# Kernel tuning notes

Hardware: AMD Instinct MI355X
Metric: run time of the kernel (lower is better)

## Reference

```python
import jax, jax.numpy as jnp
import numpy as np

N_MIN = 16
N_TABLES = 16
PER_LEVEL_SCALE = 1.3195079565048218
MAX_TABLE = 2 ** 19
H1, H2, H3 = 1, 2654435761, 805459861
OFFS = np.array([[0,0,0],[0,0,1],[0,1,0],[0,1,1],[1,0,0],[1,0,1],[1,1,0],[1,1,1]], dtype=np.int32)

def _levels():
    N_l, sizes, max_direct = [], [], 0
    for i in range(N_TABLES):
        res = int(np.ceil(N_MIN * np.exp(i * np.log(PER_LEVEL_SCALE)) - 1.0)) + 1
        ts = res ** 3
        ts = ts if ts % 8 == 0 else ((ts + 7) // 8) * 8
        ts = min(MAX_TABLE, ts)
        if ts == res ** 3:
            max_direct = i
        N_l.append(res); sizes.append(ts)
    return N_l, sizes, max_direct

N_L, SIZES, MAX_DIRECT = _levels()

def hash_encode(pos, grids):
    # pos: [N,3] in [0,1); grids: [16, MAX_TABLE, 2] (levels padded to MAX_TABLE)
    feats = []
    for l in range(N_TABLES):
        uvz = pos * jnp.float32(N_L[l])
        iuv_f = jnp.floor(uvz)
        f = uvz - iuv_f                                   # fractional part [N,3]
        corners = iuv_f.astype(jnp.int32)[:, None, :] + OFFS[None]  # [N,8,3]
        if l <= MAX_DIRECT:
            R = N_L[l]
            idx = (corners[..., 2] * (R * R) + corners[..., 1] * R + corners[..., 0]) % SIZES[l]
        else:
            cu = corners.astype(jnp.uint32)
            h = (cu[..., 0] * jnp.uint32(H1)) ^ (cu[..., 1] * jnp.uint32(H2)) ^ (cu[..., 2] * jnp.uint32(H3))
            idx = (h % jnp.uint32(SIZES[l])).astype(jnp.int32)
        c = grids[l][idx]                                 # gather -> [N,8,2]
        fx, fy, fz = f[:, 0:1], f[:, 1:2], f[:, 2:3]
        c00 = c[:, 0] * (1 - fx) + c[:, 4] * fx
        c01 = c[:, 1] * (1 - fx) + c[:, 5] * fx
        c10 = c[:, 2] * (1 - fx) + c[:, 6] * fx
        c11 = c[:, 3] * (1 - fx) + c[:, 7] * fx
        c0 = c00 * (1 - fy) + c10 * fy
        c1 = c01 * (1 - fy) + c11 * fy
        feats.append(c0 * (1 - fz) + c1 * fy)  # NOTE: c1*fy (not fz) replicates source exactly
    return jnp.concatenate(feats, axis=-1)  # [N, 32]

def setup_inputs():
    key = jax.random.key(0)
    ks = jax.random.split(key, 7)
    N = 1048576  # max_samples(512) * batch_size(2048)
    x = jax.random.uniform(ks[0], (N, 19), dtype=jnp.float32)  # pos(3) in [0,1) + dir feats(16)
    grids = (jax.random.uniform(ks[1], (N_TABLES, MAX_TABLE, 2), dtype=jnp.float32) * 2.0 - 1.0) * 1e-4
    h = 64
    w_sigma1 = jax.random.normal(ks[2], (32, h), dtype=jnp.float32) / np.sqrt(32).astype(np.float32)
    w_sigma2 = jax.random.normal(ks[3], (h, 16), dtype=jnp.float32) / np.sqrt(h).astype(np.float32)
    w_c1 = jax.random.normal(ks[4], (32, h), dtype=jnp.float32) / np.sqrt(32).astype(np.float32)
    w_c2 = jax.random.normal(ks[5], (h, h), dtype=jnp.float32) / np.sqrt(h).astype(np.float32)
    w_c3 = jax.random.normal(ks[6], (h, 3), dtype=jnp.float32) / np.sqrt(h).astype(np.float32)
    return {"x": x, "grids": grids, "w_sigma1": w_sigma1, "w_sigma2": w_sigma2,
            "w_c1": w_c1, "w_c2": w_c2, "w_c3": w_c3}

def reference(x, grids, w_sigma1, w_sigma2, w_c1, w_c2, w_c3):
    pos, direc = x[:, :3], x[:, 3:]
    enc = hash_encode(pos, grids)                       # [N,32]
    out = jax.nn.relu(enc @ w_sigma1) @ w_sigma2        # [N,16]
    sigma = out[:, 0]
    ci = jnp.concatenate([direc, out], axis=-1)         # [N,32]
    color = jax.nn.sigmoid(jax.nn.relu(jax.nn.relu(ci @ w_c1) @ w_c2) @ w_c3)  # [N,3]
    return jnp.concatenate([color, sigma[:, None]], axis=-1)  # [N,4]
```

## Files before the change

kernel.cpp:

```cpp
#include <hip/hip_runtime.h>
#include <math.h>


#define BLOCK 256
#define NTAB  (16*524288)
#define PITCH 88

constexpr int      kNL[16] = {16,22,28,37,49,65,85,112,148,195,257,338,446,589,777,1025};
constexpr unsigned kSZ[16] = {4096u,10648u,21952u,50656u,117656u,274632u,
                              524288u,524288u,524288u,524288u,524288u,
                              524288u,524288u,524288u,524288u,524288u};

typedef __attribute__((ext_vector_type(8))) short short8;
typedef __attribute__((ext_vector_type(4))) float float4v;

__device__ __forceinline__ short f2bf(float f) {
    unsigned u = __float_as_uint(f);
    unsigned r = u + 0x7fffu + ((u >> 16) & 1u);
    return (short)(r >> 16);
}
__device__ __forceinline__ float bf2f(short h) {
    return __uint_as_float(((unsigned)(unsigned short)h) << 16);
}
__device__ __forceinline__ unsigned pk2(float a, float b) {
    return ((unsigned)(unsigned short)f2bf(b) << 16) | (unsigned)(unsigned short)f2bf(a);
}
__device__ __forceinline__ float pe0(unsigned u) { return __uint_as_float(u << 16); }
__device__ __forceinline__ float pe1(unsigned u) { return __uint_as_float(u & 0xffff0000u); }

__device__ __forceinline__ unsigned trilerp_pack(const unsigned* vv, float fx, float fy, float fz)
{
    const float w0x = 1.f-fx, w0y = 1.f-fy, w0z = 1.f-fz;
    float e0, e1;
    {
        float c00 = pe0(vv[0])*w0x + pe0(vv[4])*fx;
        float c01 = pe0(vv[1])*w0x + pe0(vv[5])*fx;
        float c10 = pe0(vv[2])*w0x + pe0(vv[6])*fx;
        float c11 = pe0(vv[3])*w0x + pe0(vv[7])*fx;
        float c0 = c00*w0y + c10*fy;
        float c1 = c01*w0y + c11*fy;
        e0 = c0*w0z + c1*fy;
    }
    {
        float c00 = pe1(vv[0])*w0x + pe1(vv[4])*fx;
        float c01 = pe1(vv[1])*w0x + pe1(vv[5])*fx;
        float c10 = pe1(vv[2])*w0x + pe1(vv[6])*fx;
        float c11 = pe1(vv[3])*w0x + pe1(vv[7])*fx;
        float c0 = c00*w0y + c10*fy;
        float c1 = c01*w0y + c11*fy;
        e1 = c0*w0z + c1*fy;
    }
    return pk2(e0, e1);
}

__global__ __launch_bounds__(BLOCK)
void prep_all(const float* __restrict__ x, const float* __restrict__ grids,
              const float* __restrict__ w1, const float* __restrict__ w2,
              const float* __restrict__ wc1, const float* __restrict__ wc2,
              const float* __restrict__ wc3,
              float4* __restrict__ pos4, unsigned* __restrict__ tbu,
              uint4* __restrict__ wf, int n, int nTabBlk, int nPosBlk)
{
    const int b = blockIdx.x;
    if (b < nTabBlk) {
        int i = b * BLOCK + threadIdx.x;
        if (i < NTAB) {
            float2 v = ((const float2*)grids)[i];
            tbu[i] = pk2(v.x, v.y);
        }
    } else if (b < nTabBlk + nPosBlk) {
        int i = (b - nTabBlk) * BLOCK + threadIdx.x;
        if (i < n) {
            const float* xr = x + (size_t)i * 19;
            pos4[i] = make_float4(xr[0], xr[1], xr[2], 0.f);
        }
    } else {
        int lane = threadIdx.x;
        if (lane < 64) {
            int cn = lane & 15, q = lane >> 4;
            auto pack8 = [](const float* src, int stride) -> uint4 {
                uint4 r;
                r.x = pk2(src[0*stride], src[1*stride]);
                r.y = pk2(src[2*stride], src[3*stride]);
                r.z = pk2(src[4*stride], src[5*stride]);
                r.w = pk2(src[6*stride], src[7*stride]);
                return r;
            };
            int f = 0;
            for (int nt = 0; nt < 4; ++nt)
                wf[(f++)*64 + lane] = pack8(w1 + (q*8)*64 + nt*16 + cn, 64);
            for (int c = 0; c < 2; ++c)
                wf[(f++)*64 + lane] = pack8(w2 + (c*32 + q*8)*16 + cn, 16);
            for (int nt = 0; nt < 4; ++nt)
                wf[(f++)*64 + lane] = pack8(wc1 + (q*8)*64 + nt*16 + cn, 64);
            for (int c = 0; c < 2; ++c)
                for (int nt = 0; nt < 4; ++nt)
                    wf[(f++)*64 + lane] = pack8(wc2 + (c*32 + q*8)*64 + nt*16 + cn, 64);
            for (int c = 0; c < 2; ++c) {
                if (cn < 3) wf[(f++)*64 + lane] = pack8(wc3 + (c*32 + q*8)*3 + cn, 3);
                else { uint4 z; z.x = z.y = z.z = z.w = 0u; wf[(f++)*64 + lane] = z; }
            }
        }
    }
}

template<int L>
__device__ __forceinline__ void gather4(const float4* __restrict__ pos4,
                                        const unsigned* __restrict__ tball,
                                        unsigned* __restrict__ encu,
                                        int n, int p0, int cnt)
{
    constexpr unsigned S = kSZ[L];
    constexpr unsigned H2c = 2654435761u, H3c = 805459861u;
    constexpr int R = kNL[L];
    (void)R;
    const unsigned* __restrict__ tbu = tball + (size_t)L * 524288u;

    unsigned vv[4][8];
    float fxa[4], fya[4], fza[4];
    #pragma unroll
    for (int q = 0; q < 4; ++q) {
        if (q >= cnt) continue;
        float4 p = pos4[p0+q];
        const float Rf = (float)kNL[L];
        float ux = p.x*Rf, uy = p.y*Rf, uz = p.z*Rf;
        float gx = floorf(ux), gy = floorf(uy), gz = floorf(uz);
        fxa[q] = ux-gx; fya[q] = uy-gy; fza[q] = uz-gz;
        int ix = (int)gx, iy = (int)gy, iz = (int)gz;

        unsigned tc[4];
        #pragma unroll
        for (int c = 0; c < 4; ++c) {
            int yb = c >> 1, zb = c & 1;
            tc[c] = (unsigned)(iy+yb)*H2c ^ (unsigned)(iz+zb)*H3c;
        }
        if ((ix & 1) == 0) {
            #pragma unroll
            for (int c = 0; c < 4; ++c) {
                unsigned idx0 = ((unsigned)ix ^ tc[c]) & (S-1u);
                uint2 pr = *(const uint2*)(tbu + (idx0 & ~1u));
                unsigned swp = idx0 & 1u;
                vv[q][c]   = swp ? pr.y : pr.x;
                vv[q][4+c] = swp ? pr.x : pr.y;
            }
        } else {
            #pragma unroll
            for (int c = 0; c < 4; ++c) {
                unsigned idx0 = ((unsigned)ix     ^ tc[c]) & (S-1u);
                unsigned idx1 = ((unsigned)(ix+1) ^ tc[c]) & (S-1u);
                vv[q][c]   = tbu[idx0];
                vv[q][4+c] = tbu[idx1];
            }
        }
    }

    unsigned pkd[4];
    #pragma unroll
    for (int q = 0; q < 4; ++q) {
        if (q >= cnt) continue;
        pkd[q] = trilerp_pack(vv[q], fxa[q], fya[q], fza[q]);
    }

    unsigned* d = encu + (size_t)L*n + p0;
    if (cnt == 4) {
        uint4 o; o.x = pkd[0]; o.y = pkd[1]; o.z = pkd[2]; o.w = pkd[3];
        *(uint4*)d = o;
    } else {
        for (int q = 0; q < cnt; ++q) d[q] = pkd[q];
    }
}

__global__ __launch_bounds__(BLOCK)
void enc_all(const float4* __restrict__ pos4, const unsigned* __restrict__ tball,
             unsigned* __restrict__ encu, int n, int byA)
{
    const int bx = blockIdx.x;
    const int by = blockIdx.y;

    if (by < byA) {
        int p0 = (by*BLOCK + threadIdx.x) * 4;
        if (p0 >= n) return;
        int cnt = min(4, n - p0);
        switch (bx) {
            case 0: gather4< 6>(pos4,tball,encu,n,p0,cnt); break;
            case 1: gather4< 7>(pos4,tball,encu,n,p0,cnt); break;
            case 2: gather4< 8>(pos4,tball,encu,n,p0,cnt); break;
            case 3: gather4< 9>(pos4,tball,encu,n,p0,cnt); break;
            case 4: gather4<10>(pos4,tball,encu,n,p0,cnt); break;
            case 5: gather4<11>(pos4,tball,encu,n,p0,cnt); break;
            case 6: gather4<12>(pos4,tball,encu,n,p0,cnt); break;
            case 7: gather4<13>(pos4,tball,encu,n,p0,cnt); break;
        }
    } else {
        int q4 = (n + 3) / 4;
        int quarter = bx & 3;
        int jb = quarter * q4;
        int je = min(n, jb + q4);
        int p0 = jb + ((by-byA)*BLOCK + threadIdx.x) * 4;
        if (p0 >= je) return;
        int cnt = min(4, je - p0);
        if (bx < 4) gather4<14>(pos4,tball,encu,n,p0,cnt);
        else        gather4<15>(pos4,tball,encu,n,p0,cnt);
    }
}

template<int LV>
__device__ __forceinline__ void enc_addr(float4 p, const unsigned* __restrict__ tball,
                                         unsigned vv[8], float& fx, float& fy, float& fz)
{
    constexpr int R = kNL[LV];
    constexpr unsigned S = kSZ[LV];
    constexpr unsigned H2c = 2654435761u, H3c = 805459861u;
    const unsigned* __restrict__ tb = tball + (size_t)LV * 524288u;
    const float Rf = (float)R;
    float ux = p.x*Rf, uy = p.y*Rf, uz = p.z*Rf;
    float gx = floorf(ux), gy = floorf(uy), gz = floorf(uz);
    fx = ux-gx; fy = uy-gy; fz = uz-gz;
    int ix = (int)gx, iy = (int)gy, iz = (int)gz;

    if (LV >= 3) {
        unsigned tc[4];
        #pragma unroll
        for (int c = 0; c < 4; ++c) {
            int yb = c >> 1, zb = c & 1;
            tc[c] = (unsigned)(iy+yb)*H2c ^ (unsigned)(iz+zb)*H3c;
        }
        if ((ix & 1) == 0) {
            #pragma unroll
            for (int c = 0; c < 4; ++c) {
                unsigned h0 = (unsigned)ix ^ tc[c];
                unsigned base = (h0 & ~1u) % S;
                uint2 pr = *(const uint2*)(tb + base);
                unsigned swp = h0 & 1u;
                vv[c]   = swp ? pr.y : pr.x;
                vv[4+c] = swp ? pr.x : pr.y;
            }
        } else {
            #pragma unroll
            for (int c = 0; c < 4; ++c) {
                vv[c]   = tb[(((unsigned)ix)     ^ tc[c]) % S];
                vv[4+c] = tb[(((unsigned)(ix+1)) ^ tc[c]) % S];
            }
        }
    } else {
        #pragma unroll
        for (int j = 0; j < 8; ++j) {
            int ox = ix + ((j>>2)&1);
            int oy = iy + ((j>>1)&1);
            int oz = iz + (j&1);
            vv[j] = tb[(unsigned)((oz*(R*R) + oy*R + ox) % (int)S)];
        }
    }
}

__device__ __forceinline__ short8 ldfrag(const uint4* __restrict__ wf, int f, int lane) {
    union { uint4 u; short8 s; } cv;
    cv.u = wf[f*64 + lane];
    return cv.s;
}

__global__ __launch_bounds__(BLOCK)
void mlp_mfma(const float* __restrict__ x,
              const float4* __restrict__ pos4,
              const unsigned* __restrict__ tbu,
              const unsigned* __restrict__ encu,
              const uint4* __restrict__ wf,
              float* __restrict__ out, int n)
{
    __shared__ unsigned short s_scr[4][2][16*PITCH];
    __shared__ float s_sig[4][16];
    __shared__ float s_col[4][16][4];
    __shared__ float s_dir[4][304];
    __shared__ unsigned s_lowB[6][64];

    const int t = threadIdx.x;
    const int lane = t & 63;
    const int wave = t >> 6;
    const int m = lane & 15;
    const int q = lane >> 4;
    const int cn = m;
    const int blk = blockIdx.x * 64;
    const int pt  = blk + wave*16 + m;
    const int ptc = pt < n ? pt : n - 1;
    const int p0w = blk + wave*16;

    const float4v zero = {0.f, 0.f, 0.f, 0.f};

    unsigned encv[4];
    #pragma unroll
    for (int i = 0; i < 4; ++i) {
        int lv = q*4 + i;
        if (lv >= 6) encv[i] = encu[(size_t)lv*n + ptc];
    }

    {
        int npts = n - p0w; if (npts > 16) npts = 16; if (npts < 0) npts = 0;
        int nfl = npts * 19;
        const float* xs = x + (size_t)p0w * 19;
        float* sd = s_dir[wave];
        #pragma unroll
        for (int it = 0; it < 5; ++it) {
            int idx = it*64 + lane;
            if (idx < nfl) sd[idx] = xs[idx];
        }
    }

    {
        int pp = blk + lane; if (pp >= n) pp = n - 1;
        float4 p = pos4[pp];
        unsigned vv[8]; float fx, fy, fz;
        switch (wave) {
            case 0:  enc_addr<0>(p, tbu, vv, fx, fy, fz); break;
            case 1:  enc_addr<1>(p, tbu, vv, fx, fy, fz); break;
            case 2:  enc_addr<2>(p, tbu, vv, fx, fy, fz); break;
            default: enc_addr<3>(p, tbu, vv, fx, fy, fz); break;
        }
        s_lowB[wave][lane] = trilerp_pack(vv, fx, fy, fz);
    }
    if (lane < 32) {
        int lv = 4 + (wave >> 1);
        int pb2 = (wave & 1)*32 + lane;
        int pp = blk + pb2; if (pp >= n) pp = n - 1;
        float4 p = pos4[pp];
        unsigned vv[8]; float fx, fy, fz;
        if (lv == 4) enc_addr<4>(p, tbu, vv, fx, fy, fz);
        else         enc_addr<5>(p, tbu, vv, fx, fy, fz);
        s_lowB[lv][pb2] = trilerp_pack(vv, fx, fy, fz);
    }
    __syncthreads();

    union { unsigned u[4]; short8 s; } a1;
    #pragma unroll
    for (int i = 0; i < 4; ++i) {
        int lv = q*4 + i;
        if (lv < 6) a1.u[i] = s_lowB[lv][wave*16 + m];
        else        a1.u[i] = encv[i];
    }

    short8 bw1[4], bw2[2], bwc1[4];
    #pragma unroll
    for (int nt = 0; nt < 4; ++nt) bw1[nt] = ldfrag(wf, nt, lane);
    #pragma unroll
    for (int c = 0; c < 2; ++c)    bw2[c]  = ldfrag(wf, 4 + c, lane);
    #pragma unroll
    for (int nt = 0; nt < 4; ++nt) bwc1[nt] = ldfrag(wf, 6 + nt, lane);

    float4v h[4];
    #pragma unroll
    for (int nt = 0; nt < 4; ++nt) {
        h[nt] = __builtin_amdgcn_mfma_f32_16x16x32_bf16(a1.s, bw1[nt], zero, 0, 0, 0);
        #pragma unroll
        for (int r = 0; r < 4; ++r) h[nt][r] = fmaxf(h[nt][r], 0.f);
    }

    unsigned short* sA = &s_scr[wave][0][0];
    unsigned short* sB = &s_scr[wave][1][0];
    #pragma unroll
    for (int nt = 0; nt < 4; ++nt)
        #pragma unroll
        for (int r = 0; r < 4; ++r)
            sA[(q*4+r)*PITCH + nt*16 + cn] = (unsigned short)f2bf(h[nt][r]);
    short8 ah[2];
    #pragma unroll
    for (int c = 0; c < 2; ++c)
        ah[c] = *(const short8*)&sA[m*PITCH + c*32 + q*8];

    float4v o = __builtin_amdgcn_mfma_f32_16x16x32_bf16(ah[0], bw2[0], zero, 0, 0, 0);
    o = __builtin_amdgcn_mfma_f32_16x16x32_bf16(ah[1], bw2[1], o, 0, 0, 0);
    if (cn == 0) {
        #pragma unroll
        for (int r = 0; r < 4; ++r) s_sig[wave][q*4+r] = o[r];
    }

    #pragma unroll
    for (int r = 0; r < 4; ++r)
        sB[(q*4+r)*PITCH + cn] = (unsigned short)f2bf(o[r]);
    short8 ov = *(const short8*)&sB[m*PITCH + (q >= 2 ? (q-2)*8 : 0)];

    union { unsigned u[4]; short8 s; } ci_hi, ci_lo;
    if (q < 2) {
        const float* sd = s_dir[wave];
        int rm = ptc - p0w; if (rm < 0) rm = 0;
        #pragma unroll
        for (int i = 0; i < 4; ++i) {
            float d0 = sd[rm*19 + 3 + q*8 + 2*i];
            float d1 = sd[rm*19 + 3 + q*8 + 2*i + 1];
            short h0 = f2bf(d0), h1 = f2bf(d1);
            ci_hi.u[i] = ((unsigned)(unsigned short)h1 << 16) | (unsigned)(unsigned short)h0;
            short l0 = f2bf(d0 - bf2f(h0)), l1 = f2bf(d1 - bf2f(h1));
            ci_lo.u[i] = ((unsigned)(unsigned short)l1 << 16) | (unsigned)(unsigned short)l0;
        }
    } else {
        ci_hi.s = ov;
        #pragma unroll
        for (int i = 0; i < 4; ++i) ci_lo.u[i] = 0u;
    }

    float4v hc[4];
    #pragma unroll
    for (int nt = 0; nt < 4; ++nt) {
        hc[nt] = __builtin_amdgcn_mfma_f32_16x16x32_bf16(ci_hi.s, bwc1[nt], zero, 0, 0, 0);
        hc[nt] = __builtin_amdgcn_mfma_f32_16x16x32_bf16(ci_lo.s, bwc1[nt], hc[nt], 0, 0, 0);
        #pragma unroll
        for (int r = 0; r < 4; ++r) hc[nt][r] = fmaxf(hc[nt][r], 0.f);
    }

    short8 bwc2[2][4], bwc3[2];
    #pragma unroll
    for (int c = 0; c < 2; ++c)
        #pragma unroll
        for (int nt = 0; nt < 4; ++nt)
            bwc2[c][nt] = ldfrag(wf, 10 + c*4 + nt, lane);
    #pragma unroll
    for (int c = 0; c < 2; ++c) bwc3[c] = ldfrag(wf, 18 + c, lane);

    #pragma unroll
    for (int nt = 0; nt < 4; ++nt)
        #pragma unroll
        for (int r = 0; r < 4; ++r) {
            float v = hc[nt][r];
            short hi = f2bf(v);
            sA[(q*4+r)*PITCH + nt*16 + cn] = (unsigned short)hi;
            sB[(q*4+r)*PITCH + nt*16 + cn] = (unsigned short)f2bf(v - bf2f(hi));
        }
    short8 ghi[2], glo[2];
    #pragma unroll
    for (int c = 0; c < 2; ++c) {
        ghi[c] = *(const short8*)&sA[m*PITCH + c*32 + q*8];
        glo[c] = *(const short8*)&sB[m*PITCH + c*32 + q*8];
    }

    float4v g[4];
    #pragma unroll
    for (int nt = 0; nt < 4; ++nt) {
        float4v acc = __builtin_amdgcn_mfma_f32_16x16x32_bf16(ghi[0], bwc2[0][nt], zero, 0, 0, 0);
        acc = __builtin_amdgcn_mfma_f32_16x16x32_bf16(glo[0], bwc2[0][nt], acc, 0, 0, 0);
        acc = __builtin_amdgcn_mfma_f32_16x16x32_bf16(ghi[1], bwc2[1][nt], acc, 0, 0, 0);
        acc = __builtin_amdgcn_mfma_f32_16x16x32_bf16(glo[1], bwc2[1][nt], acc, 0, 0, 0);
        #pragma unroll
        for (int r = 0; r < 4; ++r) acc[r] = fmaxf(acc[r], 0.f);
        g[nt] = acc;
    }

    #pragma unroll
    for (int nt = 0; nt < 4; ++nt)
        #pragma unroll
        for (int r = 0; r < 4; ++r) {
            float v = g[nt][r];
            short hi = f2bf(v);
            sA[(q*4+r)*PITCH + nt*16 + cn] = (unsigned short)hi;
            sB[(q*4+r)*PITCH + nt*16 + cn] = (unsigned short)f2bf(v - bf2f(hi));
        }
    short8 uhi[2], ulo[2];
    #pragma unroll
    for (int c = 0; c < 2; ++c) {
        uhi[c] = *(const short8*)&sA[m*PITCH + c*32 + q*8];
        ulo[c] = *(const short8*)&sB[m*PITCH + c*32 + q*8];
    }

    float4v col = __builtin_amdgcn_mfma_f32_16x16x32_bf16(uhi[0], bwc3[0], zero, 0, 0, 0);
    col = __builtin_amdgcn_mfma_f32_16x16x32_bf16(ulo[0], bwc3[0], col, 0, 0, 0);
    col = __builtin_amdgcn_mfma_f32_16x16x32_bf16(uhi[1], bwc3[1], col, 0, 0, 0);
    col = __builtin_amdgcn_mfma_f32_16x16x32_bf16(ulo[1], bwc3[1], col, 0, 0, 0);
    #pragma unroll
    for (int r = 0; r < 4; ++r)
        col[r] = 1.f / (1.f + __expf(-col[r]));

    if (cn < 3) {
        #pragma unroll
        for (int r = 0; r < 4; ++r) s_col[wave][q*4+r][cn] = col[r];
    }

    __builtin_amdgcn_s_waitcnt(0);
    int pfi = lane >> 2, c4 = lane & 3;
    int pout = blk + wave*16 + pfi;
    if (pout < n) {
        float v = (c4 == 3) ? s_sig[wave][pfi] : s_col[wave][pfi][c4];
        out[(size_t)pout*4 + c4] = v;
    }
}

extern "C" void kernel_launch(void* const* d_in, const int* in_sizes, int n_in,
                              void* d_out, int out_size, void* d_ws, size_t ws_size,
                              hipStream_t stream) {
    const float* x     = (const float*)d_in[0];
    const float* grids = (const float*)d_in[1];
    const float* w1    = (const float*)d_in[2];
    const float* w2    = (const float*)d_in[3];
    const float* wc1   = (const float*)d_in[4];
    const float* wc2   = (const float*)d_in[5];
    const float* wc3   = (const float*)d_in[6];
    float* out = (float*)d_out;

    int n = in_sizes[0] / 19;
    size_t encB = (size_t)16 * n * sizeof(unsigned);
    size_t posB = (size_t)n * sizeof(float4);
    size_t tabB = (size_t)NTAB * sizeof(unsigned);

    char* p = (char*)d_ws;
    unsigned* encu = (unsigned*)p;
    float4*   pos4 = (float4*)(p + encB);
    unsigned* tbu  = (unsigned*)(p + encB + posB);
    uint4*    wf   = (uint4*)(p + encB + posB + tabB);

    int nTabBlk = (NTAB + BLOCK - 1) / BLOCK;
    int nPosBlk = (n + BLOCK - 1) / BLOCK;
    prep_all<<<nTabBlk + nPosBlk + 1, BLOCK, 0, stream>>>(
        x, grids, w1, w2, wc1, wc2, wc3, pos4, tbu, wf, n, nTabBlk, nPosBlk);

    int byA = (n + BLOCK*4 - 1) / (BLOCK*4);
    int q4  = (n + 3) / 4;
    int byB = (q4 + BLOCK*4 - 1) / (BLOCK*4);
    dim3 ge(8, byA + byB);
    enc_all<<<ge, BLOCK, 0, stream>>>(pos4, tbu, encu, n, byA);

    mlp_mfma<<<(n + 63) / 64, BLOCK, 0, stream>>>(x, pos4, tbu, encu, wf, out, n);
}
```

Baseline: 532.4 us.

## Vectorize table pack, load dir features directly, shrink LDS pitch, use HIP bf16

The grid-table packing in prep_all now handles two table entries per thread using float4 loads and uint2 stores, halving the number of table blocks. In mlp_mfma the per-wave shared-memory staging of the direction features is removed; each lane instead reads its 8 direction floats straight from global memory. The LDS pitch drops from 88 to 72, and f2bf now uses the HIP __float2bfloat16 intrinsic instead of manual rounding. Together these aim to cut prep-kernel instruction count and mlp LDS use and pressure, at the risk of uncoalesced strided global loads and new LDS bank conflicts at the smaller pitch.

```diff
diff --git a/kernel.cpp b/kernel.cpp
--- a/kernel.cpp
+++ b/kernel.cpp
@@ -1,10 +1,11 @@
 #include <hip/hip_runtime.h>
+#include <hip/hip_bf16.h>
 #include <math.h>
 
 
 #define BLOCK 256
 #define NTAB  (16*524288)
-#define PITCH 88
+#define PITCH 72
 
 constexpr int      kNL[16] = {16,22,28,37,49,65,85,112,148,195,257,338,446,589,777,1025};
 constexpr unsigned kSZ[16] = {4096u,10648u,21952u,50656u,117656u,274632u,
@@ -15,9 +16,9 @@
 typedef __attribute__((ext_vector_type(4))) float float4v;
 
 __device__ __forceinline__ short f2bf(float f) {
-    unsigned u = __float_as_uint(f);
-    unsigned r = u + 0x7fffu + ((u >> 16) & 1u);
-    return (short)(r >> 16);
+    __hip_bfloat16 h = __float2bfloat16(f);
+    union { __hip_bfloat16 b; short s; } cv; cv.b = h;
+    return cv.s;
 }
 __device__ __forceinline__ float bf2f(short h) {
     return __uint_as_float(((unsigned)(unsigned short)h) << 16);
@@ -64,9 +65,12 @@
     const int b = blockIdx.x;
     if (b < nTabBlk) {
         int i = b * BLOCK + threadIdx.x;
-        if (i < NTAB) {
-            float2 v = ((const float2*)grids)[i];
-            tbu[i] = pk2(v.x, v.y);
+        if (i < NTAB/2) {
+            float4 v = ((const float4*)grids)[i];
+            uint2 o;
+            o.x = pk2(v.x, v.y);
+            o.y = pk2(v.z, v.w);
+            ((uint2*)tbu)[i] = o;
         }
     } else if (b < nTabBlk + nPosBlk) {
         int i = (b - nTabBlk) * BLOCK + threadIdx.x;
@@ -112,8 +116,6 @@
 {
     constexpr unsigned S = kSZ[L];
     constexpr unsigned H2c = 2654435761u, H3c = 805459861u;
-    constexpr int R = kNL[L];
-    (void)R;
     const unsigned* __restrict__ tbu = tball + (size_t)L * 524288u;
 
     unsigned vv[4][8];
@@ -270,7 +272,6 @@
     __shared__ unsigned short s_scr[4][2][16*PITCH];
     __shared__ float s_sig[4][16];
     __shared__ float s_col[4][16][4];
-    __shared__ float s_dir[4][304];
     __shared__ unsigned s_lowB[6][64];
 
     const int t = threadIdx.x;
@@ -282,7 +283,6 @@
     const int blk = blockIdx.x * 64;
     const int pt  = blk + wave*16 + m;
     const int ptc = pt < n ? pt : n - 1;
-    const int p0w = blk + wave*16;
 
     const float4v zero = {0.f, 0.f, 0.f, 0.f};
 
@@ -292,17 +292,11 @@
         int lv = q*4 + i;
         if (lv >= 6) encv[i] = encu[(size_t)lv*n + ptc];
     }
-
-    {
-        int npts = n - p0w; if (npts > 16) npts = 16; if (npts < 0) npts = 0;
-        int nfl = npts * 19;
-        const float* xs = x + (size_t)p0w * 19;
-        float* sd = s_dir[wave];
-        #pragma unroll
-        for (int it = 0; it < 5; ++it) {
-            int idx = it*64 + lane;
-            if (idx < nfl) sd[idx] = xs[idx];
-        }
+    float dv[8];
+    if (q < 2) {
+        #pragma unroll
+        for (int i = 0; i < 8; ++i)
+            dv[i] = x[(size_t)ptc*19 + 3 + q*8 + i];
     }
 
     {
@@ -379,12 +373,10 @@
 
     union { unsigned u[4]; short8 s; } ci_hi, ci_lo;
     if (q < 2) {
-        const float* sd = s_dir[wave];
-        int rm = ptc - p0w; if (rm < 0) rm = 0;
         #pragma unroll
         for (int i = 0; i < 4; ++i) {
-            float d0 = sd[rm*19 + 3 + q*8 + 2*i];
-            float d1 = sd[rm*19 + 3 + q*8 + 2*i + 1];
+            float d0 = dv[2*i];
+            float d1 = dv[2*i + 1];
             short h0 = f2bf(d0), h1 = f2bf(d1);
             ci_hi.u[i] = ((unsigned)(unsigned short)h1 << 16) | (unsigned)(unsigned short)h0;
             short l0 = f2bf(d0 - bf2f(h0)), l1 = f2bf(d1 - bf2f(h1));
@@ -503,7 +495,7 @@
     unsigned* tbu  = (unsigned*)(p + encB + posB);
     uint4*    wf   = (uint4*)(p + encB + posB + tabB);
 
-    int nTabBlk = (NTAB + BLOCK - 1) / BLOCK;
+    int nTabBlk = (NTAB/2 + BLOCK - 1) / BLOCK;
     int nPosBlk = (n + BLOCK - 1) / BLOCK;
     prep_all<<<nTabBlk + nPosBlk + 1, BLOCK, 0, stream>>>(
         x, grids, w1, w2, wc1, wc2, wc3, pos4, tbu, wf, n, nTabBlk, nPosBlk);
```

Result: faster. 516.3 us (-3.0%).
